# Optimization experiments

Measured on AMD Instinct MI355X. Metric: run time of the kernel, lower is better.

Reference implementation:

```python
import jax, jax.numpy as jnp
import numpy as np

B, S, D = 4, 4096, 1024   # batch, seq, d_model
E, H = 16, 128            # n_experts, expert_size; v_dim = D


def setup_inputs() -> dict:
    key = jax.random.key(0)
    k0, k1, k2, k3 = jax.random.split(key, 4)
    std = 1.0 / np.sqrt(D)
    input_tensor = jax.random.normal(k0, (B, S, D), dtype=jnp.float32)
    expert_sel = jax.random.normal(k1, (E, D), dtype=jnp.float32) * std
    keys = jax.random.normal(k2, (E, D, H), dtype=jnp.float32) * std
    values = jax.random.normal(k3, (E, H, D), dtype=jnp.float32) * (1.0 / np.sqrt(E * H))
    return {"input_tensor": input_tensor, "expert_sel": expert_sel,
            "keys": keys, "values": values}


def reference(input_tensor, expert_sel, keys, values):
    # Router: sigmoid gate per expert. Note: the original topk selects ALL
    # routed experts (k=routed_expert_number) and then appends the shared
    # experts, so sel_index is a full permutation of all experts per token;
    # the gathered weights make the combine order-invariant. Faithful math:
    #   out = sum_e sigmoid(x @ W_sel^T)[..., e] * relu(x @ K_e) @ V_e
    sel = jax.nn.sigmoid(jnp.einsum('bsd,ed->bse', input_tensor, expert_sel))  # [B,S,E]
    scores = jax.nn.relu(jnp.einsum('bsd,edh->bseh', input_tensor, keys))       # [B,S,E,H]
    out = jnp.einsum('bseh,ehv,bse->bsv', scores, values, sel)                   # [B,S,D]
    return out
```

## Files before the change

kernel.cpp:

```cpp
#include <hip/hip_runtime.h>
#include <hip/hip_bf16.h>


typedef __attribute__((ext_vector_type(8))) short bf16x8;
typedef __attribute__((ext_vector_type(4))) float f32x4;

#define D_MODEL 1024
#define NTOK    16384
#define NEXP    16
#define HEXP    128
#define NEH     2048

__device__ __forceinline__ unsigned short f2b(float f) {
  union { float f; unsigned u; } c; c.f = f;
  unsigned u = c.u;
  return (unsigned short)((u + 0x7FFFu + ((u >> 16) & 1u)) >> 16);
}

__device__ __forceinline__ void gload16(const void* g, void* l) {
  __builtin_amdgcn_global_load_lds(
      (const __attribute__((address_space(1))) void*)g,
      (__attribute__((address_space(3))) void*)l,
      16, 0, 0);
}


__global__ void cvt_x_kernel(const float4* __restrict__ x, ushort4* __restrict__ o) {
  int i = blockIdx.x * 256 + threadIdx.x;
  float4 v = x[i];
  ushort4 r;
  r.x = f2b(v.x); r.y = f2b(v.y); r.z = f2b(v.z); r.w = f2b(v.w);
  o[i] = r;
}

__global__ void cvt_es_kernel(const float4* __restrict__ es, ushort4* __restrict__ o) {
  int i = blockIdx.x * 256 + threadIdx.x;
  float4 v = es[i];
  ushort4 r;
  r.x = f2b(v.x); r.y = f2b(v.y); r.z = f2b(v.z); r.w = f2b(v.w);
  o[i] = r;
}

__global__ void cvt_keys_kernel(const float* __restrict__ k, unsigned short* __restrict__ kt) {
  int idx = blockIdx.x * 256 + threadIdx.x;
  int d  = idx & 1023;
  int eh = idx >> 10;
  int h  = eh & 127;
  int e  = eh >> 7;
  kt[idx] = f2b(k[(e << 17) + (d << 7) + h]);
}

__global__ void cvt_vals_kernel(const float* __restrict__ v, unsigned short* __restrict__ vt) {
  int idx = blockIdx.x * 256 + threadIdx.x;
  int eh = idx & 2047;
  int d  = idx >> 11;
  int e  = eh >> 7;
  int h  = eh & 127;
  vt[idx] = f2b(v[(e << 17) + (h << 10) + d]);
}

__global__ __launch_bounds__(256)
void sel_mfma_kernel(const unsigned short* __restrict__ Xb,
                     const unsigned short* __restrict__ ESb,
                     float* __restrict__ sel) {
  const int wave = threadIdx.x >> 6;
  const int lane = threadIdx.x & 63;
  const int tk = blockIdx.x * 64 + wave * 16;
  const int lr = lane & 15;
  const int hk = (lane >> 4) * 8;

  const unsigned short* a0 = Xb + (size_t)(tk + lr) * D_MODEL + hk;
  const unsigned short* b0 = ESb + (size_t)lr * D_MODEL + hk;

  f32x4 acc = {};
#pragma unroll
  for (int k0 = 0; k0 < D_MODEL; k0 += 32) {
    bf16x8 a = *(const bf16x8*)(a0 + k0);
    bf16x8 b = *(const bf16x8*)(b0 + k0);
    acc = __builtin_amdgcn_mfma_f32_16x16x32_bf16(a, b, acc, 0, 0, 0);
  }

  const int r0 = tk + (lane >> 4) * 4;
#pragma unroll
  for (int j = 0; j < 4; ++j)
    sel[(size_t)(r0 + j) * NEXP + lr] = 1.f / (1.f + __expf(-acc[j]));
}

template <int EPI>
__global__ __launch_bounds__(256, 3)
void gemm_bt(const unsigned short* __restrict__ A, const unsigned short* __restrict__ Bt,
             int K, int N, const float* __restrict__ sel,
             unsigned short* __restrict__ outB, float* __restrict__ outF) {
  __shared__ unsigned short As[128 * 64];
  __shared__ unsigned short Bs[128 * 64];

  const int tid  = threadIdx.x;
  const int wave = tid >> 6;
  const int lane = tid & 63;
  const int brow = blockIdx.x * 128;
  const int bcol = blockIdx.y * 128;
  const int wr = (wave >> 1) * 64;
  const int wc = (wave & 1) * 64;
  const int lr = lane & 15;
  const int lk = (lane >> 4) * 8;

  f32x4 acc[4][4] = {};

  const unsigned short* aPtr = A + (size_t)(brow + (tid >> 3)) * K + (tid & 7) * 8;
  const unsigned short* bPtr = Bt + (size_t)(bcol + (tid >> 3)) * K + (tid & 7) * 8;
  char* asW = (char*)As + (wave << 10);
  char* bsW = (char*)Bs + (wave << 10);

  for (int k0 = 0; k0 < K; k0 += 64) {
#pragma unroll
    for (int i = 0; i < 4; ++i) {
      gload16(aPtr + (size_t)i * 32 * K, asW + i * 4096);
      gload16(bPtr + (size_t)i * 32 * K, bsW + i * 4096);
    }
    aPtr += 64;
    bPtr += 64;
    __syncthreads();
#pragma unroll
    for (int kk = 0; kk < 2; ++kk) {
      bf16x8 a[4], b[4];
#pragma unroll
      for (int m = 0; m < 4; ++m)
        a[m] = *(const bf16x8*)&As[(wr + m * 16 + lr) * 64 + kk * 32 + lk];
#pragma unroll
      for (int n = 0; n < 4; ++n)
        b[n] = *(const bf16x8*)&Bs[(wc + n * 16 + lr) * 64 + kk * 32 + lk];
#pragma unroll
      for (int m = 0; m < 4; ++m)
#pragma unroll
        for (int n = 0; n < 4; ++n)
          acc[m][n] = __builtin_amdgcn_mfma_f32_16x16x32_bf16(a[m], b[n], acc[m][n], 0, 0, 0);
    }
    __syncthreads();
  }

  const int r0 = brow + wr + (lane >> 4) * 4;
  const int c0 = bcol + wc + lr;

  if (EPI == 0) {
    const int e = bcol >> 7;
#pragma unroll
    for (int m = 0; m < 4; ++m) {
#pragma unroll
      for (int j = 0; j < 4; ++j) {
        const int r = r0 + m * 16 + j;
        const float s = sel[r * NEXP + e];
#pragma unroll
        for (int n = 0; n < 4; ++n) {
          float v = acc[m][n][j];
          v = v > 0.f ? v * s : 0.f;
          outB[(size_t)r * N + c0 + n * 16] = f2b(v);
        }
      }
    }
  } else {
#pragma unroll
    for (int m = 0; m < 4; ++m) {
#pragma unroll
      for (int j = 0; j < 4; ++j) {
        const int r = r0 + m * 16 + j;
#pragma unroll
        for (int n = 0; n < 4; ++n)
          outF[(size_t)r * N + c0 + n * 16] = acc[m][n][j];
      }
    }
  }
}


extern "C" void kernel_launch(void* const* d_in, const int* in_sizes, int n_in,
                              void* d_out, int out_size, void* d_ws, size_t ws_size,
                              hipStream_t stream) {
  const float* X  = (const float*)d_in[0];
  const float* ES = (const float*)d_in[1];
  const float* Kw = (const float*)d_in[2];
  const float* Vw = (const float*)d_in[3];
  float* out = (float*)d_out;

  char* ws = (char*)d_ws;
  unsigned short* Xb  = (unsigned short*)ws; ws += (size_t)NTOK * D_MODEL * 2;
  unsigned short* Sc  = (unsigned short*)ws; ws += (size_t)NTOK * NEH * 2;
  unsigned short* Kt  = (unsigned short*)ws; ws += (size_t)NEH * D_MODEL * 2;
  unsigned short* Vt  = (unsigned short*)ws; ws += (size_t)D_MODEL * NEH * 2;
  unsigned short* ESb = (unsigned short*)ws; ws += (size_t)NEXP * D_MODEL * 2;
  float*          Sl  = (float*)ws;          ws += (size_t)NTOK * NEXP * 4;

  cvt_x_kernel<<<NTOK * D_MODEL / 4 / 256, 256, 0, stream>>>((const float4*)X, (ushort4*)Xb);
  cvt_es_kernel<<<NEXP * D_MODEL / 4 / 256, 256, 0, stream>>>((const float4*)ES, (ushort4*)ESb);
  cvt_keys_kernel<<<NEH * D_MODEL / 256, 256, 0, stream>>>(Kw, Kt);
  cvt_vals_kernel<<<D_MODEL * NEH / 256, 256, 0, stream>>>(Vw, Vt);

  sel_mfma_kernel<<<NTOK / 64, 256, 0, stream>>>(Xb, ESb, Sl);

  dim3 g1(NTOK / 128, NEH / 128);
  gemm_bt<0><<<g1, 256, 0, stream>>>(Xb, Kt, D_MODEL, NEH, Sl, Sc, nullptr);

  dim3 g2(NTOK / 128, D_MODEL / 128);
  gemm_bt<1><<<g2, 256, 0, stream>>>(Sc, Vt, NEH, D_MODEL, nullptr, nullptr, out);
}
```

Measured before the change: 344.9 us.

## Rewrite GEMMs as 256x256 tiles with triple-buffered async LDS pipeline

Replaces the 128x128, 256-thread GEMM with a 256x256, 512-thread kernel that has a 3-stage LDS ring of 32-wide K slices loaded via global_load_lds. Loads run two stages ahead, with explicit vmcnt waits. Adds an XOR swizzle to cut LDS bank conflicts and raises wave priority around the MFMA block. The goal is more data reuse per tile and load latency hidden behind compute. The cost is higher register pressure (8x4 accumulators) and fewer blocks in the grid.

```diff
diff --git a/kernel.cpp b/kernel.cpp
--- a/kernel.cpp
+++ b/kernel.cpp
@@ -8,7 +8,6 @@
 #define D_MODEL 1024
 #define NTOK    16384
 #define NEXP    16
-#define HEXP    128
 #define NEH     2048
 
 __device__ __forceinline__ unsigned short f2b(float f) {
@@ -87,85 +86,115 @@
 }
 
 template <int EPI>
-__global__ __launch_bounds__(256, 3)
-void gemm_bt(const unsigned short* __restrict__ A, const unsigned short* __restrict__ Bt,
+__global__ __launch_bounds__(512, 2)
+void gemm256(const unsigned short* __restrict__ A, const unsigned short* __restrict__ Bt,
              int K, int N, const float* __restrict__ sel,
              unsigned short* __restrict__ outB, float* __restrict__ outF) {
-  __shared__ unsigned short As[128 * 64];
-  __shared__ unsigned short Bs[128 * 64];
+  __shared__ char lds[3 * 32768];
 
   const int tid  = threadIdx.x;
   const int wave = tid >> 6;
   const int lane = tid & 63;
-  const int brow = blockIdx.x * 128;
-  const int bcol = blockIdx.y * 128;
-  const int wr = (wave >> 1) * 64;
-  const int wc = (wave & 1) * 64;
-  const int lr = lane & 15;
-  const int lk = (lane >> 4) * 8;
-
-  f32x4 acc[4][4] = {};
-
-  const unsigned short* aPtr = A + (size_t)(brow + (tid >> 3)) * K + (tid & 7) * 8;
-  const unsigned short* bPtr = Bt + (size_t)(bcol + (tid >> 3)) * K + (tid & 7) * 8;
-  char* asW = (char*)As + (wave << 10);
-  char* bsW = (char*)Bs + (wave << 10);
-
-  for (int k0 = 0; k0 < K; k0 += 64) {
-#pragma unroll
-    for (int i = 0; i < 4; ++i) {
-      gload16(aPtr + (size_t)i * 32 * K, asW + i * 4096);
-      gload16(bPtr + (size_t)i * 32 * K, bsW + i * 4096);
+  const int wrow = wave >> 2;
+  const int wcol = wave & 3;
+  const int lr   = lane & 15;
+  const int brow = blockIdx.x << 8;
+  const int bcol = blockIdx.y << 8;
+
+  const int r0 = tid >> 2,          g0 = (tid & 3) ^ (r0 & 3);
+  const int r1 = (512 + tid) >> 2,  g1 = (tid & 3) ^ (r1 & 3);
+  const unsigned short* aS0 = A  + (size_t)(brow + r0) * K + g0 * 8;
+  const unsigned short* aS1 = A  + (size_t)(brow + r1) * K + g1 * 8;
+  const unsigned short* bS0 = Bt + (size_t)(bcol + r0) * K + g0 * 8;
+  const unsigned short* bS1 = Bt + (size_t)(bcol + r1) * K + g1 * 8;
+  const int dW = wave << 10;
+
+  const int swz = (((lane >> 4) ^ (lr & 3)) << 4);
+  int aOff[8], bOff[4];
+#pragma unroll
+  for (int m = 0; m < 8; ++m)
+    aOff[m] = (wrow * 128 + m * 16 + lr) * 64 + swz;
+#pragma unroll
+  for (int n = 0; n < 4; ++n)
+    bOff[n] = 16384 + (wcol * 64 + n * 16 + lr) * 64 + swz;
+
+  f32x4 acc[8][4] = {};
+  const int nt = K >> 5;
+
+#define STAGEK(t, b) {                                          \
+    char* base_ = lds + (b) * 32768;                            \
+    gload16(aS0 + (size_t)(t) * 32, base_ + dW);                \
+    gload16(aS1 + (size_t)(t) * 32, base_ + 8192 + dW);         \
+    gload16(bS0 + (size_t)(t) * 32, base_ + 16384 + dW);        \
+    gload16(bS1 + (size_t)(t) * 32, base_ + 24576 + dW);        \
+  }
+
+  STAGEK(0, 0);
+  STAGEK(1, 1);
+
+  int cur = 0, stg = 2;
+  for (int t = 0; t < nt; ++t) {
+    if (t + 2 < nt) {
+      STAGEK(t + 2, stg);
+      asm volatile("s_waitcnt vmcnt(8)" ::: "memory");
+    } else if (t + 2 == nt) {
+      asm volatile("s_waitcnt vmcnt(4)" ::: "memory");
+    } else {
+      asm volatile("s_waitcnt vmcnt(0)" ::: "memory");
     }
-    aPtr += 64;
-    bPtr += 64;
-    __syncthreads();
-#pragma unroll
-    for (int kk = 0; kk < 2; ++kk) {
-      bf16x8 a[4], b[4];
-#pragma unroll
-      for (int m = 0; m < 4; ++m)
-        a[m] = *(const bf16x8*)&As[(wr + m * 16 + lr) * 64 + kk * 32 + lk];
+    __builtin_amdgcn_s_barrier();
+    asm volatile("" ::: "memory");
+
+    const char* buf = lds + cur * 32768;
+    bf16x8 a[8], b[4];
+#pragma unroll
+    for (int m = 0; m < 8; ++m) a[m] = *(const bf16x8*)(buf + aOff[m]);
+#pragma unroll
+    for (int n = 0; n < 4; ++n) b[n] = *(const bf16x8*)(buf + bOff[n]);
+
+    __builtin_amdgcn_s_setprio(1);
+#pragma unroll
+    for (int m = 0; m < 8; ++m)
 #pragma unroll
       for (int n = 0; n < 4; ++n)
-        b[n] = *(const bf16x8*)&Bs[(wc + n * 16 + lr) * 64 + kk * 32 + lk];
-#pragma unroll
-      for (int m = 0; m < 4; ++m)
-#pragma unroll
-        for (int n = 0; n < 4; ++n)
-          acc[m][n] = __builtin_amdgcn_mfma_f32_16x16x32_bf16(a[m], b[n], acc[m][n], 0, 0, 0);
-    }
-    __syncthreads();
-  }
-
-  const int r0 = brow + wr + (lane >> 4) * 4;
-  const int c0 = bcol + wc + lr;
+        acc[m][n] = __builtin_amdgcn_mfma_f32_16x16x32_bf16(a[m], b[n], acc[m][n], 0, 0, 0);
+    __builtin_amdgcn_s_setprio(0);
+
+    asm volatile("s_waitcnt lgkmcnt(0)" ::: "memory");
+    __builtin_amdgcn_s_barrier();
+    cur = (cur == 2) ? 0 : cur + 1;
+    stg = (stg == 2) ? 0 : stg + 1;
+  }
+#undef STAGEK
+
+  const int rb = brow + wrow * 128 + ((lane >> 4) << 2);
+  const int cb = bcol + (wcol << 6) + lr;
 
   if (EPI == 0) {
-    const int e = bcol >> 7;
-#pragma unroll
-    for (int m = 0; m < 4; ++m) {
+    const int e = (bcol >> 7) + (wcol >> 1);
+#pragma unroll
+    for (int m = 0; m < 8; ++m) {
 #pragma unroll
       for (int j = 0; j < 4; ++j) {
-        const int r = r0 + m * 16 + j;
-        const float s = sel[r * NEXP + e];
+        const int r = rb + m * 16 + j;
+        const float s = sel[(size_t)r * NEXP + e];
 #pragma unroll
         for (int n = 0; n < 4; ++n) {
           float v = acc[m][n][j];
           v = v > 0.f ? v * s : 0.f;
-          outB[(size_t)r * N + c0 + n * 16] = f2b(v);
+          outB[(size_t)r * N + cb + n * 16] = f2b(v);
         }
       }
     }
   } else {
 #pragma unroll
-    for (int m = 0; m < 4; ++m) {
+    for (int m = 0; m < 8; ++m) {
 #pragma unroll
       for (int j = 0; j < 4; ++j) {
-        const int r = r0 + m * 16 + j;
+        const int r = rb + m * 16 + j;
 #pragma unroll
         for (int n = 0; n < 4; ++n)
-          outF[(size_t)r * N + c0 + n * 16] = acc[m][n][j];
+          outF[(size_t)r * N + cb + n * 16] = acc[m][n][j];
       }
     }
   }
@@ -196,9 +225,9 @@
 
   sel_mfma_kernel<<<NTOK / 64, 256, 0, stream>>>(Xb, ESb, Sl);
 
-  dim3 g1(NTOK / 128, NEH / 128);
-  gemm_bt<0><<<g1, 256, 0, stream>>>(Xb, Kt, D_MODEL, NEH, Sl, Sc, nullptr);
-
-  dim3 g2(NTOK / 128, D_MODEL / 128);
-  gemm_bt<1><<<g2, 256, 0, stream>>>(Sc, Vt, NEH, D_MODEL, nullptr, nullptr, out);
-}
+  dim3 g1(NTOK / 256, NEH / 256);
+  gemm256<0><<<g1, 512, 0, stream>>>(Xb, Kt, D_MODEL, NEH, Sl, Sc, nullptr);
+
+  dim3 g2(NTOK / 256, D_MODEL / 256);
+  gemm256<1><<<g2, 512, 0, stream>>>(Sc, Vt, NEH, D_MODEL, nullptr, nullptr, out);
+}
```

Measured after the change: 307.0 us. 1.12x faster.
